# Performance work log

Measured on AMD Instinct MI355X. Metric: run time of the kernel, lower is better.

Reference implementation:

```python
import jax, jax.numpy as jnp
import numpy as np

B, T, N, F_IN = 32, 64, 128, 16
H, SOUT = 64, 16
D = N * SOUT            # transformer d_model = 2048
NHEADS, DH = 16, 128
DFF, LAYERS = 2048, 2
NCLASSES, OUT = 8, 10
THR = 0.004             # edge threshold on sigmoid(V)/N


def setup_inputs():
    key = jax.random.key(0)
    ks = iter(jax.random.split(key, 40))
    r = lambda *s: jax.random.normal(next(ks), s, jnp.float32) * 0.02
    return {
        'X': jax.random.normal(next(ks), (B, T, N * F_IN), jnp.float32),
        'V_Adap': jax.random.normal(next(ks), (NCLASSES, N, N), jnp.float32),
        'Wl': r(F_IN, H), 'bl': jnp.zeros((H,)),
        'Wr': r(F_IN, H), 'br': jnp.zeros((H,)),
        'att': jax.random.normal(next(ks), (H,), jnp.float32) * 0.1,
        'gat_bias': jnp.zeros((H,)),
        'Wfc': r(H, SOUT), 'bfc': jnp.zeros((SOUT,)),
        'Wq': r(LAYERS, D, D), 'bq': jnp.zeros((LAYERS, D)),
        'Wk': r(LAYERS, D, D), 'bk': jnp.zeros((LAYERS, D)),
        'Wv': r(LAYERS, D, D), 'bv': jnp.zeros((LAYERS, D)),
        'Wo': r(LAYERS, D, D), 'bo': jnp.zeros((LAYERS, D)),
        'ln1_g': jnp.ones((LAYERS, D)), 'ln1_b': jnp.zeros((LAYERS, D)),
        'W1': r(LAYERS, D, DFF), 'b1': jnp.zeros((LAYERS, DFF)),
        'W2': r(LAYERS, DFF, D), 'b2': jnp.zeros((LAYERS, D)),
        'ln2_g': jnp.ones((LAYERS, D)), 'ln2_b': jnp.zeros((LAYERS, D)),
        'Wout': r(D, OUT), 'bout': jnp.zeros((OUT,)),
        'class_idx': 2,
    }


def _ln(x, g, b):
    mu = jnp.mean(x, -1, keepdims=True)
    var = jnp.var(x, -1, keepdims=True)
    return (x - mu) / jnp.sqrt(var + 1e-5) * g + b


def reference(X, V_Adap, Wl, bl, Wr, br, att, gat_bias, Wfc, bfc,
              Wq, bq, Wk, bk, Wv, bv, Wo, bo, ln1_g, ln1_b,
              W1, b1, W2, b2, ln2_g, ln2_b, Wout, bout, class_idx):
    # dynamic adjacency: sigmoid + scale + threshold (data-dependent sparsity as a mask)
    A = jax.nn.sigmoid(V_Adap[class_idx]) / N
    mask = (A > THR) | jnp.eye(N, dtype=bool)   # GATv2Conv default add_self_loops

    def gat_step(x_t):                           # x_t: (B, N, F_IN)
        xl = x_t @ Wl + bl                       # source transform (B, N, H)
        xr = x_t @ Wr + br                       # target transform (B, N, H)
        s = jax.nn.leaky_relu(xl[:, :, None, :] + xr[:, None, :, :], 0.2)  # (B, src, dst, H)
        e = jnp.where(mask[None], jnp.einsum('bijh,h->bij', s, att), -1e9)
        alpha = jax.nn.softmax(e, axis=1)        # softmax over sources per target node
        out = jnp.einsum('bij,bih->bjh', alpha, xl) + gat_bias
        return out @ Wfc + bfc                   # (B, N, SOUT)

    Xr = X.reshape(B, T, N, F_IN).transpose(1, 0, 2, 3)   # (T, B, N, F)
    spatial = jax.lax.map(gat_step, Xr)                   # (T, B, N, SOUT)
    h = spatial.transpose(1, 0, 2, 3).reshape(B, T, D)

    # post-norm TransformerEncoder (torch defaults: relu, d_ff=2048, no dropout at eval)
    for l in range(LAYERS):
        q = (h @ Wq[l] + bq[l]).reshape(B, T, NHEADS, DH).transpose(0, 2, 1, 3)
        k = (h @ Wk[l] + bk[l]).reshape(B, T, NHEADS, DH).transpose(0, 2, 1, 3)
        v = (h @ Wv[l] + bv[l]).reshape(B, T, NHEADS, DH).transpose(0, 2, 1, 3)
        aw = jax.nn.softmax(jnp.einsum('bhqd,bhkd->bhqk', q, k) / np.float32(np.sqrt(DH)), axis=-1)
        ao = jnp.einsum('bhqk,bhkd->bhqd', aw, v).transpose(0, 2, 1, 3).reshape(B, T, D)
        h = _ln(h + ao @ Wo[l] + bo[l], ln1_g[l], ln1_b[l])
        ff = jax.nn.relu(h @ W1[l] + b1[l]) @ W2[l] + b2[l]
        h = _ln(h + ff, ln2_g[l], ln2_b[l])

    return h[:, -1, :] @ Wout + bout             # (B, OUT)
```

## Files before the change

### kernel.cpp

```cpp
#include <hip/hip_runtime.h>
#include <cstdint>
#include <cstddef>


typedef unsigned short u16;
typedef __bf16 bf16x8 __attribute__((ext_vector_type(8)));
typedef float f32x4 __attribute__((ext_vector_type(4)));
typedef unsigned int u32x4 __attribute__((ext_vector_type(4)));
typedef float f32x4v __attribute__((ext_vector_type(4)));
typedef unsigned short u16x4 __attribute__((ext_vector_type(4)));

__device__ __forceinline__ u16 f2b(float f) {
  union { float f; unsigned u; } x; x.f = f;
  unsigned r = x.u + 0x7fffu + ((x.u >> 16) & 1u);
  return (u16)(r >> 16);
}
__device__ __forceinline__ float b2f(u16 s) {
  union { unsigned u; float f; } x; x.u = ((unsigned)s) << 16;
  return x.f;
}
__device__ __forceinline__ float b2f_lo(unsigned q) {
  union { unsigned u; float f; } x; x.u = q << 16;
  return x.f;
}
__device__ __forceinline__ float b2f_hi(unsigned q) {
  union { unsigned u; float f; } x; x.u = q & 0xffff0000u;
  return x.f;
}

__device__ __forceinline__ void gload_lds16(const void* g, void* l) {
  __builtin_amdgcn_global_load_lds(
      (const __attribute__((address_space(1))) unsigned int*)g,
      (__attribute__((address_space(3))) unsigned int*)l, 16, 0, 0);
}

__global__ __launch_bounds__(1024) void gat_kernel(
    const float* __restrict__ X, const float* __restrict__ V_Adap,
    const int* __restrict__ class_idx,
    const float* __restrict__ Wl, const float* __restrict__ bl,
    const float* __restrict__ Wr, const float* __restrict__ br,
    const float* __restrict__ att, const float* __restrict__ gat_bias,
    const float* __restrict__ Wfc, const float* __restrict__ bfc,
    float* __restrict__ h_f32, u16* __restrict__ h_b16)
{
  const int bt = blockIdx.x;
  const int tid = threadIdx.x;

  __shared__ __align__(16) float xlT[64 * 132];
  __shared__ __align__(16) float xrT[64 * 132];
  __shared__ __align__(16) u16   xlTb[64 * 136];
  __shared__ __align__(16) u16   esbT[128 * 136];
  __shared__ __align__(16) u16   aggb[128 * 72];
  __shared__ __align__(16) float WlT[64 * 20];
  __shared__ __align__(16) float WrT[64 * 20];
  __shared__ __align__(16) float WfcT[16 * 66];
  __shared__ float atts[64], bls[64], brs[64], gbias[64], bfcs[16];
  __shared__ float cls[128], crs[128], inv_s[128];
  __shared__ float red[8 * 128];

  {
    const int h = tid >> 4, f = tid & 15;
    WlT[h * 20 + f] = Wl[f * 64 + h];
    WrT[h * 20 + f] = Wr[f * 64 + h];
    WfcT[f * 66 + h] = Wfc[h * 16 + f];
  }
  if (tid < 64) { atts[tid] = att[tid]; bls[tid] = bl[tid]; brs[tid] = br[tid]; gbias[tid] = gat_bias[tid]; }
  if (tid < 16) bfcs[tid] = bfc[tid];
  const int cidx = *class_idx;
  __syncthreads();

  {
    const int n = tid >> 3, hq = tid & 7;
    const float* xp = X + (size_t)bt * 2048 + n * 16;
    float xv[16];
    #pragma unroll
    for (int f4 = 0; f4 < 4; f4++) {
      f32x4v t4 = ((const f32x4v*)xp)[f4];
      xv[f4 * 4 + 0] = t4[0]; xv[f4 * 4 + 1] = t4[1];
      xv[f4 * 4 + 2] = t4[2]; xv[f4 * 4 + 3] = t4[3];
    }
    #pragma unroll
    for (int k = 0; k < 8; k++) {
      const int h = hq + 8 * k;
      float al = bls[h], ar = brs[h];
      #pragma unroll
      for (int f4 = 0; f4 < 4; f4++) {
        f32x4v wl = *(const f32x4v*)&WlT[h * 20 + f4 * 4];
        f32x4v wr = *(const f32x4v*)&WrT[h * 20 + f4 * 4];
        #pragma unroll
        for (int f = 0; f < 4; f++) {
          al = fmaf(xv[f4 * 4 + f], wl[f], al);
          ar = fmaf(xv[f4 * 4 + f], wr[f], ar);
        }
      }
      xlT[h * 132 + n] = al;
      xrT[h * 132 + n] = ar;
      xlTb[h * 136 + n] = f2b(al);
    }
  }
  __syncthreads();

  if (tid < 256) {
    const int n = tid & 127;
    const float* srcT = (tid < 128) ? xlT : xrT;
    float s = 0.f;
    for (int h = 0; h < 64; h++) s = fmaf(atts[h], srcT[h * 132 + n], s);
    if (tid < 128) cls[n] = s; else crs[n] = s;
  }
  __syncthreads();

  {
    const int i0 = (tid >> 5) * 4;
    const int j0 = (tid & 31) * 4;
    float acc[4][4] = {};
    #pragma unroll 2
    for (int h = 0; h < 64; h++) {
      const float ah = atts[h];
      f32x4v xa = *(const f32x4v*)&xlT[h * 132 + i0];
      f32x4v xb = *(const f32x4v*)&xrT[h * 132 + j0];
      #pragma unroll
      for (int a = 0; a < 4; a++)
        #pragma unroll
        for (int b = 0; b < 4; b++)
          acc[a][b] = fmaf(ah, __builtin_fabsf(xa[a] + xb[b]), acc[a][b]);
    }
    const float* Vc = V_Adap + (size_t)cidx * 16384;
    float vm[4][4];
    #pragma unroll
    for (int a = 0; a < 4; a++) {
      f32x4v vc = *(const f32x4v*)&Vc[(size_t)(i0 + a) * 128 + j0];
      #pragma unroll
      for (int b = 0; b < 4; b++) vm[a][b] = vc[b];
    }
    #pragma unroll
    for (int b = 0; b < 4; b++) {
      const int j = j0 + b;
      const float ej = 0.6f * crs[j];
      u16x4 pk;
      #pragma unroll
      for (int a = 0; a < 4; a++) {
        const int i = i0 + a;
        const float e = ej + 0.6f * cls[i] + 0.4f * acc[a][b];
        const bool m = (vm[a][b] > 0.04800922f) || (i == j);
        pk[a] = f2b(m ? e : -1e9f);
      }
      *(u16x4*)&esbT[j * 136 + i0] = pk;
    }
  }
  __syncthreads();

  {
    const int j = tid >> 3, c = tid & 7;
    u16* rp = &esbT[j * 136 + c * 16];
    float ps = 0.f;
    #pragma unroll
    for (int half = 0; half < 2; half++) {
      u32x4 q = *(u32x4*)(rp + half * 8);
      #pragma unroll
      for (int w2 = 0; w2 < 4; w2++) {
        const float p0 = __expf(b2f_lo(q[w2]));
        const float p1 = __expf(b2f_hi(q[w2]));
        ps += p0 + p1;
        q[w2] = (unsigned)f2b(p0) | ((unsigned)f2b(p1) << 16);
      }
      *(u32x4*)(rp + half * 8) = q;
    }
    red[c * 128 + j] = ps;
  }
  __syncthreads();
  if (tid < 128) {
    float s = 0.f;
    #pragma unroll
    for (int c = 0; c < 8; c++) s += red[c * 128 + tid];
    inv_s[tid] = 1.f / s;
  }
  __syncthreads();

  {
    const int w = tid >> 6, lane = tid & 63;
    const int lq = lane >> 4, lr = lane & 15;
    const int jt = w >> 1, ht0 = (w & 1) * 2;
    f32x4 acc2[2] = {};
    #pragma unroll
    for (int ks = 0; ks < 4; ks++) {
      const bf16x8 af = __builtin_bit_cast(bf16x8,
          *(const u32x4*)&esbT[(jt * 16 + lr) * 136 + ks * 32 + lq * 8]);
      #pragma unroll
      for (int t = 0; t < 2; t++) {
        const bf16x8 bfb = __builtin_bit_cast(bf16x8,
            *(const u32x4*)&xlTb[((ht0 + t) * 16 + lr) * 136 + ks * 32 + lq * 8]);
        acc2[t] = __builtin_amdgcn_mfma_f32_16x16x32_bf16(af, bfb, acc2[t], 0, 0, 0);
      }
    }
    #pragma unroll
    for (int t = 0; t < 2; t++) {
      const int h = (ht0 + t) * 16 + lr;
      const float gb = gbias[h];
      #pragma unroll
      for (int r = 0; r < 4; r++) {
        const int j = jt * 16 + lq * 4 + r;
        aggb[j * 72 + h] = f2b(acc2[t][r] * inv_s[j] + gb);
      }
    }
  }
  __syncthreads();

  {
    const int j = tid >> 3, s0 = (tid & 7) * 2;
    float o0 = bfcs[s0], o1 = bfcs[s0 + 1];
    #pragma unroll
    for (int h8 = 0; h8 < 8; h8++) {
      u32x4 q = *(const u32x4*)&aggb[j * 72 + h8 * 8];
      #pragma unroll
      for (int w2 = 0; w2 < 4; w2++) {
        const int h = h8 * 8 + w2 * 2;
        const float a0 = b2f_lo(q[w2]);
        const float a1 = b2f_hi(q[w2]);
        o0 = fmaf(a0, WfcT[s0 * 66 + h], o0);
        o1 = fmaf(a0, WfcT[(s0 + 1) * 66 + h], o1);
        o0 = fmaf(a1, WfcT[s0 * 66 + h + 1], o0);
        o1 = fmaf(a1, WfcT[(s0 + 1) * 66 + h + 1], o1);
      }
    }
    const size_t off = (size_t)bt * 2048 + j * 16 + s0;
    h_f32[off] = o0; h_f32[off + 1] = o1;
    h_b16[off] = f2b(o0); h_b16[off + 1] = f2b(o1);
  }
}

struct TransArgs {
  const float* s0; const float* s1; const float* s2;
  u16* d0; u16* d1; u16* d2;
};

__global__ __launch_bounds__(256) void transpose_cast(TransArgs p)
{
  const float* src = (blockIdx.z == 0) ? p.s0 : (blockIdx.z == 1) ? p.s1 : p.s2;
  u16* dst = (blockIdx.z == 0) ? p.d0 : (blockIdx.z == 1) ? p.d1 : p.d2;
  __shared__ u16 tile[64][66];
  const int k0 = blockIdx.y * 64, n0 = blockIdx.x * 64;
  const int tid = threadIdx.x;
  const int c = tid & 63, rb = tid >> 6;
  #pragma unroll
  for (int r = 0; r < 16; r++) {
    const int k = rb + r * 4;
    tile[k][c] = f2b(src[(size_t)(k0 + k) * 2048 + n0 + c]);
  }
  __syncthreads();
  #pragma unroll
  for (int r = 0; r < 16; r++) {
    const int n = rb + r * 4;
    dst[(size_t)(n0 + n) * 2048 + k0 + c] = tile[c][n];
  }
}

struct GemmArgs {
  const u16* A;
  const u16* Bt0; const u16* Bt1; const u16* Bt2;
  const float* b0; const float* b1; const float* b2;
  void* C0; void* C1; void* C2;
  int N; int K;
};

template <int MODE>
__global__ __launch_bounds__(256) void gemm_bt(GemmArgs g)
{
  const int z = blockIdx.z;
  const u16* Bt = (z == 0) ? g.Bt0 : (z == 1) ? g.Bt1 : g.Bt2;
  const float* bias = (z == 0) ? g.b0 : (z == 1) ? g.b1 : g.b2;
  void* C = (z == 0) ? g.C0 : (z == 1) ? g.C1 : g.C2;
  const int N = g.N, K = g.K;
  const int m0 = blockIdx.y * 128, n0 = blockIdx.x * 128;

  __shared__ __align__(16) u16 As[128 * 32];
  __shared__ __align__(16) u16 Bs[128 * 32];

  const int tid = threadIdx.x;
  const int lane = tid & 63, w = tid >> 6;
  const int srow = w * 16 + (lane >> 2);
  const int scol = (lane & 3) * 8;
  const u16* gA = g.A + (size_t)(m0 + srow) * K + scol;
  const u16* gB = Bt + (size_t)(n0 + srow) * K + scol;
  u16* lA0 = &As[(w * 16) * 32];
  u16* lA1 = &As[(64 + w * 16) * 32];
  u16* lB0 = &Bs[(w * 16) * 32];
  u16* lB1 = &Bs[(64 + w * 16) * 32];

  const int wm = (w >> 1) * 64, wn = (w & 1) * 64;
  const int lq = lane >> 4, lr = lane & 15;

  f32x4 acc[4][4] = {};

  for (int k0 = 0; k0 < K; k0 += 32) {
    gload_lds16(gA + k0, lA0);
    gload_lds16(gA + (size_t)64 * K + k0, lA1);
    gload_lds16(gB + k0, lB0);
    gload_lds16(gB + (size_t)64 * K + k0, lB1);
    __syncthreads();

    bf16x8 af[4], bf[4];
    #pragma unroll
    for (int i = 0; i < 4; i++) {
      af[i] = __builtin_bit_cast(bf16x8, *(const u32x4*)&As[(wm + i * 16 + lr) * 32 + lq * 8]);
      bf[i] = __builtin_bit_cast(bf16x8, *(const u32x4*)&Bs[(wn + i * 16 + lr) * 32 + lq * 8]);
    }
    #pragma unroll
    for (int mi = 0; mi < 4; mi++)
      #pragma unroll
      for (int ni = 0; ni < 4; ni++)
        acc[mi][ni] = __builtin_amdgcn_mfma_f32_16x16x32_bf16(af[mi], bf[ni], acc[mi][ni], 0, 0, 0);
    __syncthreads();
  }

  #pragma unroll
  for (int ni = 0; ni < 4; ni++) {
    const int col = n0 + wn + ni * 16 + lr;
    const float bv = bias[col];
    #pragma unroll
    for (int mi = 0; mi < 4; mi++) {
      #pragma unroll
      for (int r = 0; r < 4; r++) {
        const int row = m0 + wm + mi * 16 + lq * 4 + r;
        float v = acc[mi][ni][r] + bv;
        if (MODE == 0) {
          ((float*)C)[(size_t)row * N + col] = v;
        } else {
          if (MODE == 2) v = fmaxf(v, 0.f);
          ((u16*)C)[(size_t)row * N + col] = f2b(v);
        }
      }
    }
  }
}

template <int MODE>
__global__ __launch_bounds__(256) void gemm_bt64(GemmArgs g)
{
  const u16* Bt = g.Bt0;
  const float* bias = g.b0;
  void* C = g.C0;
  const int N = g.N, K = g.K;
  const int m0 = blockIdx.y * 128, n0 = blockIdx.x * 64;

  __shared__ __align__(16) u16 As[128 * 32];
  __shared__ __align__(16) u16 Bs[64 * 32];

  const int tid = threadIdx.x;
  const int lane = tid & 63, w = tid >> 6;
  const int srow = w * 16 + (lane >> 2);
  const int scol = (lane & 3) * 8;
  const u16* gA = g.A + (size_t)(m0 + srow) * K + scol;
  const u16* gB = Bt + (size_t)(n0 + srow) * K + scol;
  u16* lA0 = &As[(w * 16) * 32];
  u16* lA1 = &As[(64 + w * 16) * 32];
  u16* lB0 = &Bs[(w * 16) * 32];

  const int wm = w * 32;
  const int lq = lane >> 4, lr = lane & 15;

  f32x4 acc[2][4] = {};

  for (int k0 = 0; k0 < K; k0 += 32) {
    gload_lds16(gA + k0, lA0);
    gload_lds16(gA + (size_t)64 * K + k0, lA1);
    gload_lds16(gB + k0, lB0);
    __syncthreads();

    bf16x8 af[2], bf[4];
    #pragma unroll
    for (int i = 0; i < 2; i++)
      af[i] = __builtin_bit_cast(bf16x8, *(const u32x4*)&As[(wm + i * 16 + lr) * 32 + lq * 8]);
    #pragma unroll
    for (int i = 0; i < 4; i++)
      bf[i] = __builtin_bit_cast(bf16x8, *(const u32x4*)&Bs[(i * 16 + lr) * 32 + lq * 8]);
    #pragma unroll
    for (int mi = 0; mi < 2; mi++)
      #pragma unroll
      for (int ni = 0; ni < 4; ni++)
        acc[mi][ni] = __builtin_amdgcn_mfma_f32_16x16x32_bf16(af[mi], bf[ni], acc[mi][ni], 0, 0, 0);
    __syncthreads();
  }

  #pragma unroll
  for (int ni = 0; ni < 4; ni++) {
    const int col = n0 + ni * 16 + lr;
    const float bv = bias[col];
    #pragma unroll
    for (int mi = 0; mi < 2; mi++) {
      #pragma unroll
      for (int r = 0; r < 4; r++) {
        const int row = m0 + wm + mi * 16 + lq * 4 + r;
        float v = acc[mi][ni][r] + bv;
        if (MODE == 0) {
          ((float*)C)[(size_t)row * N + col] = v;
        } else {
          if (MODE == 2) v = fmaxf(v, 0.f);
          ((u16*)C)[(size_t)row * N + col] = f2b(v);
        }
      }
    }
  }
}

__global__ __launch_bounds__(256) void attn_kernel(
    const u16* __restrict__ Qb, const u16* __restrict__ Kb,
    const u16* __restrict__ Vb, u16* __restrict__ AOb)
{
  const int head = blockIdx.x, b = blockIdx.y;
  const int tid = threadIdx.x;
  __shared__ __align__(16) float qs[64 * 129];
  __shared__ __align__(16) float ks[64 * 129];
  __shared__ __align__(16) float vs[64 * 128];
  __shared__ __align__(16) float ss[64 * 65];
  const size_t base = ((size_t)b * 64) * 2048 + (size_t)head * 128;

  for (int idx = tid; idx < 8192; idx += 256) {
    const int t_ = idx >> 7, d = idx & 127;
    const size_t gp = base + (size_t)t_ * 2048 + d;
    qs[t_ * 129 + d] = b2f(Qb[gp]);
    ks[t_ * 129 + d] = b2f(Kb[gp]);
    vs[t_ * 128 + d] = b2f(Vb[gp]);
  }
  __syncthreads();

  {
    const int i0 = (tid >> 4) * 4, j0 = (tid & 15) * 4;
    float acc[4][4] = {};
    for (int d = 0; d < 128; d++) {
      float qv[4], kv[4];
      #pragma unroll
      for (int a = 0; a < 4; a++) qv[a] = qs[(i0 + a) * 129 + d];
      #pragma unroll
      for (int c = 0; c < 4; c++) kv[c] = ks[(j0 + c) * 129 + d];
      #pragma unroll
      for (int a = 0; a < 4; a++)
        #pragma unroll
        for (int c = 0; c < 4; c++)
          acc[a][c] = fmaf(qv[a], kv[c], acc[a][c]);
    }
    const float sc = 0.08838834764831845f;
    #pragma unroll
    for (int a = 0; a < 4; a++)
      #pragma unroll
      for (int c = 0; c < 4; c++)
        ss[(i0 + a) * 65 + j0 + c] = acc[a][c] * sc;
  }
  __syncthreads();

  if (tid < 64) {
    float mx = -3e38f;
    for (int j = 0; j < 64; j++) mx = fmaxf(mx, ss[tid * 65 + j]);
    float s = 0.f;
    for (int j = 0; j < 64; j++) {
      const float p = __expf(ss[tid * 65 + j] - mx);
      ss[tid * 65 + j] = p; s += p;
    }
    const float inv = 1.f / s;
    for (int j = 0; j < 64; j++) ss[tid * 65 + j] *= inv;
  }
  __syncthreads();

  {
    const int i0 = (tid >> 4) * 4, d0 = (tid & 15) * 8;
    float o[4][8] = {};
    for (int j = 0; j < 64; j++) {
      float pv[4];
      #pragma unroll
      for (int a = 0; a < 4; a++) pv[a] = ss[(i0 + a) * 65 + j];
      f32x4v v0 = *(const f32x4v*)&vs[j * 128 + d0];
      f32x4v v1 = *(const f32x4v*)&vs[j * 128 + d0 + 4];
      float vv[8] = {v0[0], v0[1], v0[2], v0[3], v1[0], v1[1], v1[2], v1[3]};
      #pragma unroll
      for (int a = 0; a < 4; a++)
        #pragma unroll
        for (int c = 0; c < 8; c++)
          o[a][c] = fmaf(pv[a], vv[c], o[a][c]);
    }
    #pragma unroll
    for (int a = 0; a < 4; a++)
      #pragma unroll
      for (int c = 0; c < 8; c++)
        AOb[base + (size_t)(i0 + a) * 2048 + d0 + c] = f2b(o[a][c]);
  }
}

__global__ __launch_bounds__(256) void ln_kernel(
    const float* __restrict__ hin, const float* __restrict__ delta,
    const float* __restrict__ gamma, const float* __restrict__ beta,
    float* __restrict__ hout, u16* __restrict__ bout_)
{
  const int token = blockIdx.x, tid = threadIdx.x;
  const size_t off = (size_t)token * 2048;
  __shared__ float red[8];
  float v[8];
  float s = 0.f;
  #pragma unroll
  for (int r = 0; r < 8; r++) {
    const int i = r * 256 + tid;
    v[r] = hin[off + i] + delta[off + i];
    s += v[r];
  }
  #pragma unroll
  for (int o = 32; o > 0; o >>= 1) s += __shfl_down(s, o, 64);
  if ((tid & 63) == 0) red[tid >> 6] = s;
  __syncthreads();
  const float mean = (red[0] + red[1] + red[2] + red[3]) * (1.f / 2048.f);
  float s2 = 0.f;
  #pragma unroll
  for (int r = 0; r < 8; r++) { const float d = v[r] - mean; s2 = fmaf(d, d, s2); }
  #pragma unroll
  for (int o = 32; o > 0; o >>= 1) s2 += __shfl_down(s2, o, 64);
  if ((tid & 63) == 0) red[4 + (tid >> 6)] = s2;
  __syncthreads();
  const float var = (red[4] + red[5] + red[6] + red[7]) * (1.f / 2048.f);
  const float rstd = rsqrtf(var + 1e-5f);
  #pragma unroll
  for (int r = 0; r < 8; r++) {
    const int i = r * 256 + tid;
    const float y = (v[r] - mean) * rstd * gamma[i] + beta[i];
    hout[off + i] = y;
    bout_[off + i] = f2b(y);
  }
}

__global__ __launch_bounds__(256) void final_kernel(
    const float* __restrict__ h, const float* __restrict__ Wout,
    const float* __restrict__ bout, float* __restrict__ out)
{
  const int b = blockIdx.x, tid = threadIdx.x;
  __shared__ float row[2048];
  __shared__ float part[256];
  const float* hr = h + ((size_t)b * 64 + 63) * 2048;
  for (int i = tid; i < 2048; i += 256) row[i] = hr[i];
  __syncthreads();
  const int o = tid & 15, ch = tid >> 4;
  float s = 0.f;
  if (o < 10) {
    const int i0 = ch * 128;
    for (int i = i0; i < i0 + 128; i++) s = fmaf(row[i], Wout[(size_t)i * 10 + o], s);
  }
  part[tid] = s;
  __syncthreads();
  if (tid < 10) {
    float t = bout[tid];
    for (int c2 = 0; c2 < 16; c2++) t += part[c2 * 16 + tid];
    out[(size_t)b * 10 + tid] = t;
  }
}

extern "C" void kernel_launch(void* const* d_in, const int* in_sizes, int n_in,
                              void* d_out, int out_size, void* d_ws, size_t ws_size,
                              hipStream_t stream)
{
  const float* X        = (const float*)d_in[0];
  const float* V_Adap   = (const float*)d_in[1];
  const float* Wl       = (const float*)d_in[2];
  const float* bl       = (const float*)d_in[3];
  const float* Wr       = (const float*)d_in[4];
  const float* br       = (const float*)d_in[5];
  const float* att      = (const float*)d_in[6];
  const float* gat_bias = (const float*)d_in[7];
  const float* Wfc      = (const float*)d_in[8];
  const float* bfc      = (const float*)d_in[9];
  const float* Wq       = (const float*)d_in[10];
  const float* bq       = (const float*)d_in[11];
  const float* Wk       = (const float*)d_in[12];
  const float* bk       = (const float*)d_in[13];
  const float* Wv       = (const float*)d_in[14];
  const float* bv       = (const float*)d_in[15];
  const float* Wo       = (const float*)d_in[16];
  const float* bo       = (const float*)d_in[17];
  const float* ln1_g    = (const float*)d_in[18];
  const float* ln1_b    = (const float*)d_in[19];
  const float* W1       = (const float*)d_in[20];
  const float* b1       = (const float*)d_in[21];
  const float* W2       = (const float*)d_in[22];
  const float* b2       = (const float*)d_in[23];
  const float* ln2_g    = (const float*)d_in[24];
  const float* ln2_b    = (const float*)d_in[25];
  const float* WoutP    = (const float*)d_in[26];
  const float* boutP    = (const float*)d_in[27];
  const int*   class_idx = (const int*)d_in[28];

  char* ws = (char*)d_ws;
  const size_t MB = (size_t)1 << 20;
  float* h_f32 = (float*)(ws);
  u16*   h_b16 = (u16*)(ws + 16 * MB);
  u16*   Qb    = (u16*)(ws + 24 * MB);
  u16*   Kb    = (u16*)(ws + 32 * MB);
  u16*   Vb    = (u16*)(ws + 40 * MB);
  u16*   AOb   = (u16*)(ws + 48 * MB);
  float* tmp   = (float*)(ws + 56 * MB);
  u16*   ff1b  = (u16*)(ws + 72 * MB);
  u16*   Wt0   = (u16*)(ws + 80 * MB);
  u16*   Wt1   = (u16*)(ws + 88 * MB);
  u16*   Wt2   = (u16*)(ws + 96 * MB);

  gat_kernel<<<2048, 1024, 0, stream>>>(X, V_Adap, class_idx, Wl, bl, Wr, br,
                                        att, gat_bias, Wfc, bfc, h_f32, h_b16);

  const size_t DD = 2048ull * 2048ull;
  for (int l = 0; l < 2; l++) {
    const size_t wofs = (size_t)l * DD;
    const size_t bofs = (size_t)l * 2048;

    transpose_cast<<<dim3(32, 32, 3), 256, 0, stream>>>(
        TransArgs{Wq + wofs, Wk + wofs, Wv + wofs, Wt0, Wt1, Wt2});
    gemm_bt<1><<<dim3(16, 16, 3), 256, 0, stream>>>(
        GemmArgs{h_b16, Wt0, Wt1, Wt2, bq + bofs, bk + bofs, bv + bofs,
                 Qb, Kb, Vb, 2048, 2048});

    attn_kernel<<<dim3(16, 32), 256, 0, stream>>>(Qb, Kb, Vb, AOb);

    transpose_cast<<<dim3(32, 32, 3), 256, 0, stream>>>(
        TransArgs{Wo + wofs, W1 + wofs, W2 + wofs, Wt0, Wt1, Wt2});

    gemm_bt64<0><<<dim3(32, 16), 256, 0, stream>>>(
        GemmArgs{AOb, Wt0, nullptr, nullptr, bo + bofs, nullptr, nullptr,
                 tmp, nullptr, nullptr, 2048, 2048});
    ln_kernel<<<2048, 256, 0, stream>>>(h_f32, tmp, ln1_g + bofs, ln1_b + bofs,
                                        h_f32, h_b16);

    gemm_bt64<2><<<dim3(32, 16), 256, 0, stream>>>(
        GemmArgs{h_b16, Wt1, nullptr, nullptr, b1 + bofs, nullptr, nullptr,
                 ff1b, nullptr, nullptr, 2048, 2048});

    gemm_bt64<0><<<dim3(32, 16), 256, 0, stream>>>(
        GemmArgs{ff1b, Wt2, nullptr, nullptr, b2 + bofs, nullptr, nullptr,
                 tmp, nullptr, nullptr, 2048, 2048});
    ln_kernel<<<2048, 256, 0, stream>>>(h_f32, tmp, ln2_g + bofs, ln2_b + bofs,
                                        h_f32, h_b16);
  }

  final_kernel<<<32, 256, 0, stream>>>(h_f32, WoutP, boutP, (float*)d_out);
}
```

Measured before the change: 966.4 us.

## Double-buffer GEMM LDS tiles with swizzle, vectorize attention and layernorm

Both bf16 GEMM kernels now double-buffer their LDS tiles, issuing the next K-tile's global-to-LDS loads before computing the current one. This removes one barrier per iteration and overlaps memory with MFMA work. Both also XOR-swizzle LDS columns to cut bank conflicts, and the 64-wide variant moves to K-tiles of 64. The attention kernel gets vectorized bf16 loads, float4 QK^T inner products, padding changed to 132, and a softmax spread over all 256 threads with shuffle reductions. The layernorm kernel uses float4 loads and stores. The cost is twice the LDS per GEMM block, which may reduce occupancy.

```diff
diff --git a/kernel.cpp b/kernel.cpp
--- a/kernel.cpp
+++ b/kernel.cpp
@@ -272,45 +272,58 @@
   const int N = g.N, K = g.K;
   const int m0 = blockIdx.y * 128, n0 = blockIdx.x * 128;
 
-  __shared__ __align__(16) u16 As[128 * 32];
-  __shared__ __align__(16) u16 Bs[128 * 32];
+  __shared__ __align__(16) u16 As[2][128 * 32];
+  __shared__ __align__(16) u16 Bs[2][128 * 32];
 
   const int tid = threadIdx.x;
   const int lane = tid & 63, w = tid >> 6;
   const int srow = w * 16 + (lane >> 2);
-  const int scol = (lane & 3) * 8;
+  const int scol = ((lane & 3) ^ ((lane >> 2) & 3)) * 8;
   const u16* gA = g.A + (size_t)(m0 + srow) * K + scol;
   const u16* gB = Bt + (size_t)(n0 + srow) * K + scol;
-  u16* lA0 = &As[(w * 16) * 32];
-  u16* lA1 = &As[(64 + w * 16) * 32];
-  u16* lB0 = &Bs[(w * 16) * 32];
-  u16* lB1 = &Bs[(64 + w * 16) * 32];
+  const int lbase = (w * 16) * 32;
 
   const int wm = (w >> 1) * 64, wn = (w & 1) * 64;
   const int lq = lane >> 4, lr = lane & 15;
+  const int csw = (lr & 3) << 3;
 
   f32x4 acc[4][4] = {};
-
-  for (int k0 = 0; k0 < K; k0 += 32) {
-    gload_lds16(gA + k0, lA0);
-    gload_lds16(gA + (size_t)64 * K + k0, lA1);
-    gload_lds16(gB + k0, lB0);
-    gload_lds16(gB + (size_t)64 * K + k0, lB1);
+  const int NT = K >> 5;
+
+  auto stage = [&](int buf, int kt) {
+    const int kk = kt << 5;
+    #pragma unroll
+    for (int c = 0; c < 2; c++) {
+      gload_lds16(gA + (size_t)(c * 64) * K + kk, &As[buf][lbase + c * 64 * 32]);
+      gload_lds16(gB + (size_t)(c * 64) * K + kk, &Bs[buf][lbase + c * 64 * 32]);
+    }
+  };
+  auto compute = [&](int buf) {
+    bf16x8 af[4], bfr[4];
+    #pragma unroll
+    for (int i = 0; i < 4; i++) {
+      af[i] = __builtin_bit_cast(bf16x8,
+          *(const u32x4*)&As[buf][(wm + i * 16 + lr) * 32 + ((lq * 8) ^ csw)]);
+      bfr[i] = __builtin_bit_cast(bf16x8,
+          *(const u32x4*)&Bs[buf][(wn + i * 16 + lr) * 32 + ((lq * 8) ^ csw)]);
+    }
+    #pragma unroll
+    for (int mi = 0; mi < 4; mi++)
+      #pragma unroll
+      for (int ni = 0; ni < 4; ni++)
+        acc[mi][ni] = __builtin_amdgcn_mfma_f32_16x16x32_bf16(af[mi], bfr[ni], acc[mi][ni], 0, 0, 0);
+  };
+
+  stage(0, 0);
+  __syncthreads();
+  int cur = 0;
+  for (int kt = 0; kt + 1 < NT; ++kt) {
+    stage(cur ^ 1, kt + 1);
+    compute(cur);
     __syncthreads();
-
-    bf16x8 af[4], bf[4];
-    #pragma unroll
-    for (int i = 0; i < 4; i++) {
-      af[i] = __builtin_bit_cast(bf16x8, *(const u32x4*)&As[(wm + i * 16 + lr) * 32 + lq * 8]);
-      bf[i] = __builtin_bit_cast(bf16x8, *(const u32x4*)&Bs[(wn + i * 16 + lr) * 32 + lq * 8]);
-    }
-    #pragma unroll
-    for (int mi = 0; mi < 4; mi++)
-      #pragma unroll
-      for (int ni = 0; ni < 4; ni++)
-        acc[mi][ni] = __builtin_amdgcn_mfma_f32_16x16x32_bf16(af[mi], bf[ni], acc[mi][ni], 0, 0, 0);
-    __syncthreads();
-  }
+    cur ^= 1;
+  }
+  compute(cur);
 
   #pragma unroll
   for (int ni = 0; ni < 4; ni++) {
@@ -342,44 +355,63 @@
   const int N = g.N, K = g.K;
   const int m0 = blockIdx.y * 128, n0 = blockIdx.x * 64;
 
-  __shared__ __align__(16) u16 As[128 * 32];
-  __shared__ __align__(16) u16 Bs[64 * 32];
+  __shared__ __align__(16) u16 As[2][128 * 64];
+  __shared__ __align__(16) u16 Bs[2][64 * 64];
 
   const int tid = threadIdx.x;
   const int lane = tid & 63, w = tid >> 6;
-  const int srow = w * 16 + (lane >> 2);
-  const int scol = (lane & 3) * 8;
+  const int srow = w * 8 + (lane >> 3);
+  const int scol = ((lane & 7) ^ (lane >> 3)) * 8;
   const u16* gA = g.A + (size_t)(m0 + srow) * K + scol;
   const u16* gB = Bt + (size_t)(n0 + srow) * K + scol;
-  u16* lA0 = &As[(w * 16) * 32];
-  u16* lA1 = &As[(64 + w * 16) * 32];
-  u16* lB0 = &Bs[(w * 16) * 32];
+  const int lbase = (w * 8) * 64;
 
   const int wm = w * 32;
   const int lq = lane >> 4, lr = lane & 15;
+  const int csw = (lr & 7) << 3;
 
   f32x4 acc[2][4] = {};
-
-  for (int k0 = 0; k0 < K; k0 += 32) {
-    gload_lds16(gA + k0, lA0);
-    gload_lds16(gA + (size_t)64 * K + k0, lA1);
-    gload_lds16(gB + k0, lB0);
+  const int NT = K >> 6;
+
+  auto stage = [&](int buf, int kt) {
+    const int kk = kt << 6;
+    #pragma unroll
+    for (int c = 0; c < 4; c++)
+      gload_lds16(gA + (size_t)(c * 32) * K + kk, &As[buf][lbase + c * 32 * 64]);
+    #pragma unroll
+    for (int c = 0; c < 2; c++)
+      gload_lds16(gB + (size_t)(c * 32) * K + kk, &Bs[buf][lbase + c * 32 * 64]);
+  };
+  auto compute = [&](int buf) {
+    #pragma unroll
+    for (int ks = 0; ks < 2; ks++) {
+      bf16x8 af[2], bfr[4];
+      #pragma unroll
+      for (int i = 0; i < 2; i++)
+        af[i] = __builtin_bit_cast(bf16x8,
+            *(const u32x4*)&As[buf][(wm + i * 16 + lr) * 64 + ((ks * 32 + lq * 8) ^ csw)]);
+      #pragma unroll
+      for (int i = 0; i < 4; i++)
+        bfr[i] = __builtin_bit_cast(bf16x8,
+            *(const u32x4*)&Bs[buf][(i * 16 + lr) * 64 + ((ks * 32 + lq * 8) ^ csw)]);
+      #pragma unroll
+      for (int mi = 0; mi < 2; mi++)
+        #pragma unroll
+        for (int ni = 0; ni < 4; ni++)
+          acc[mi][ni] = __builtin_amdgcn_mfma_f32_16x16x32_bf16(af[mi], bfr[ni], acc[mi][ni], 0, 0, 0);
+    }
+  };
+
+  stage(0, 0);
+  __syncthreads();
+  int cur = 0;
+  for (int kt = 0; kt + 1 < NT; ++kt) {
+    stage(cur ^ 1, kt + 1);
+    compute(cur);
     __syncthreads();
-
-    bf16x8 af[2], bf[4];
-    #pragma unroll
-    for (int i = 0; i < 2; i++)
-      af[i] = __builtin_bit_cast(bf16x8, *(const u32x4*)&As[(wm + i * 16 + lr) * 32 + lq * 8]);
-    #pragma unroll
-    for (int i = 0; i < 4; i++)
-      bf[i] = __builtin_bit_cast(bf16x8, *(const u32x4*)&Bs[(i * 16 + lr) * 32 + lq * 8]);
-    #pragma unroll
-    for (int mi = 0; mi < 2; mi++)
-      #pragma unroll
-      for (int ni = 0; ni < 4; ni++)
-        acc[mi][ni] = __builtin_amdgcn_mfma_f32_16x16x32_bf16(af[mi], bf[ni], acc[mi][ni], 0, 0, 0);
-    __syncthreads();
-  }
+    cur ^= 1;
+  }
+  compute(cur);
 
   #pragma unroll
   for (int ni = 0; ni < 4; ni++) {
@@ -408,55 +440,73 @@
 {
   const int head = blockIdx.x, b = blockIdx.y;
   const int tid = threadIdx.x;
-  __shared__ __align__(16) float qs[64 * 129];
-  __shared__ __align__(16) float ks[64 * 129];
+  __shared__ __align__(16) float qs[64 * 132];
+  __shared__ __align__(16) float ks[64 * 132];
   __shared__ __align__(16) float vs[64 * 128];
   __shared__ __align__(16) float ss[64 * 65];
   const size_t base = ((size_t)b * 64) * 2048 + (size_t)head * 128;
 
-  for (int idx = tid; idx < 8192; idx += 256) {
-    const int t_ = idx >> 7, d = idx & 127;
-    const size_t gp = base + (size_t)t_ * 2048 + d;
-    qs[t_ * 129 + d] = b2f(Qb[gp]);
-    ks[t_ * 129 + d] = b2f(Kb[gp]);
-    vs[t_ * 128 + d] = b2f(Vb[gp]);
-  }
-  __syncthreads();
-
-  {
-    const int i0 = (tid >> 4) * 4, j0 = (tid & 15) * 4;
+  for (int idx = tid; idx < 1024; idx += 256) {
+    const int t_ = idx >> 4, d8 = (idx & 15) * 8;
+    const size_t gp = base + (size_t)t_ * 2048 + d8;
+    const u32x4 q = *(const u32x4*)(Qb + gp);
+    const u32x4 k = *(const u32x4*)(Kb + gp);
+    const u32x4 v = *(const u32x4*)(Vb + gp);
+    f32x4 q0 = {b2f_lo(q[0]), b2f_hi(q[0]), b2f_lo(q[1]), b2f_hi(q[1])};
+    f32x4 q1 = {b2f_lo(q[2]), b2f_hi(q[2]), b2f_lo(q[3]), b2f_hi(q[3])};
+    f32x4 k0 = {b2f_lo(k[0]), b2f_hi(k[0]), b2f_lo(k[1]), b2f_hi(k[1])};
+    f32x4 k1 = {b2f_lo(k[2]), b2f_hi(k[2]), b2f_lo(k[3]), b2f_hi(k[3])};
+    f32x4 v0 = {b2f_lo(v[0]), b2f_hi(v[0]), b2f_lo(v[1]), b2f_hi(v[1])};
+    f32x4 v1 = {b2f_lo(v[2]), b2f_hi(v[2]), b2f_lo(v[3]), b2f_hi(v[3])};
+    *(f32x4*)&qs[t_ * 132 + d8] = q0; *(f32x4*)&qs[t_ * 132 + d8 + 4] = q1;
+    *(f32x4*)&ks[t_ * 132 + d8] = k0; *(f32x4*)&ks[t_ * 132 + d8 + 4] = k1;
+    *(f32x4*)&vs[t_ * 128 + d8] = v0; *(f32x4*)&vs[t_ * 128 + d8 + 4] = v1;
+  }
+  __syncthreads();
+
+  {
+    const int i0 = (tid >> 4) * 4, j0 = tid & 15;
     float acc[4][4] = {};
-    for (int d = 0; d < 128; d++) {
-      float qv[4], kv[4];
-      #pragma unroll
-      for (int a = 0; a < 4; a++) qv[a] = qs[(i0 + a) * 129 + d];
-      #pragma unroll
-      for (int c = 0; c < 4; c++) kv[c] = ks[(j0 + c) * 129 + d];
+    #pragma unroll 2
+    for (int d0 = 0; d0 < 128; d0 += 4) {
+      f32x4 qv[4], kv[4];
+      #pragma unroll
+      for (int a = 0; a < 4; a++) qv[a] = *(const f32x4*)&qs[(i0 + a) * 132 + d0];
+      #pragma unroll
+      for (int c = 0; c < 4; c++) kv[c] = *(const f32x4*)&ks[(j0 + c * 16) * 132 + d0];
       #pragma unroll
       for (int a = 0; a < 4; a++)
         #pragma unroll
         for (int c = 0; c < 4; c++)
-          acc[a][c] = fmaf(qv[a], kv[c], acc[a][c]);
+          #pragma unroll
+          for (int e = 0; e < 4; e++)
+            acc[a][c] = fmaf(qv[a][e], kv[c][e], acc[a][c]);
     }
     const float sc = 0.08838834764831845f;
     #pragma unroll
     for (int a = 0; a < 4; a++)
       #pragma unroll
       for (int c = 0; c < 4; c++)
-        ss[(i0 + a) * 65 + j0 + c] = acc[a][c] * sc;
-  }
-  __syncthreads();
-
-  if (tid < 64) {
+        ss[(i0 + a) * 65 + j0 + c * 16] = acc[a][c] * sc;
+  }
+  __syncthreads();
+
+  {
+    const int row = tid >> 2;
+    float* rp = &ss[row * 65 + (tid & 3) * 16];
     float mx = -3e38f;
-    for (int j = 0; j < 64; j++) mx = fmaxf(mx, ss[tid * 65 + j]);
+    #pragma unroll
+    for (int j = 0; j < 16; j++) mx = fmaxf(mx, rp[j]);
+    mx = fmaxf(mx, __shfl_xor(mx, 1, 64));
+    mx = fmaxf(mx, __shfl_xor(mx, 2, 64));
     float s = 0.f;
-    for (int j = 0; j < 64; j++) {
-      const float p = __expf(ss[tid * 65 + j] - mx);
-      ss[tid * 65 + j] = p; s += p;
-    }
+    #pragma unroll
+    for (int j = 0; j < 16; j++) { const float p = __expf(rp[j] - mx); rp[j] = p; s += p; }
+    s += __shfl_xor(s, 1, 64);
+    s += __shfl_xor(s, 2, 64);
     const float inv = 1.f / s;
-    for (int j = 0; j < 64; j++) ss[tid * 65 + j] *= inv;
+    #pragma unroll
+    for (int j = 0; j < 16; j++) rp[j] *= inv;
   }
   __syncthreads();
 
@@ -492,13 +542,15 @@
   const int token = blockIdx.x, tid = threadIdx.x;
   const size_t off = (size_t)token * 2048;
   __shared__ float red[8];
-  float v[8];
+  f32x4 v[2];
   float s = 0.f;
   #pragma unroll
-  for (int r = 0; r < 8; r++) {
-    const int i = r * 256 + tid;
-    v[r] = hin[off + i] + delta[off + i];
-    s += v[r];
+  for (int r = 0; r < 2; r++) {
+    const int i = r * 1024 + tid * 4;
+    const f32x4 a = *(const f32x4*)(hin + off + i);
+    const f32x4 b = *(const f32x4*)(delta + off + i);
+    v[r] = a + b;
+    s += v[r][0] + v[r][1] + v[r][2] + v[r][3];
   }
   #pragma unroll
   for (int o = 32; o > 0; o >>= 1) s += __shfl_down(s, o, 64);
@@ -507,7 +559,9 @@
   const float mean = (red[0] + red[1] + red[2] + red[3]) * (1.f / 2048.f);
   float s2 = 0.f;
   #pragma unroll
-  for (int r = 0; r < 8; r++) { const float d = v[r] - mean; s2 = fmaf(d, d, s2); }
+  for (int r = 0; r < 2; r++)
+    #pragma unroll
+    for (int e = 0; e < 4; e++) { const float d = v[r][e] - mean; s2 = fmaf(d, d, s2); }
   #pragma unroll
   for (int o = 32; o > 0; o >>= 1) s2 += __shfl_down(s2, o, 64);
   if ((tid & 63) == 0) red[4 + (tid >> 6)] = s2;
@@ -515,11 +569,19 @@
   const float var = (red[4] + red[5] + red[6] + red[7]) * (1.f / 2048.f);
   const float rstd = rsqrtf(var + 1e-5f);
   #pragma unroll
-  for (int r = 0; r < 8; r++) {
-    const int i = r * 256 + tid;
-    const float y = (v[r] - mean) * rstd * gamma[i] + beta[i];
-    hout[off + i] = y;
-    bout_[off + i] = f2b(y);
+  for (int r = 0; r < 2; r++) {
+    const int i = r * 1024 + tid * 4;
+    const f32x4 gm = *(const f32x4*)(gamma + i);
+    const f32x4 bt = *(const f32x4*)(beta + i);
+    f32x4 y;
+    u16x4 pb;
+    #pragma unroll
+    for (int e = 0; e < 4; e++) {
+      y[e] = (v[r][e] - mean) * rstd * gm[e] + bt[e];
+      pb[e] = f2b(y[e]);
+    }
+    *(f32x4*)(hout + off + i) = y;
+    *(u16x4*)(bout_ + off + i) = pb;
   }
 }
 
```

New measurement: 907.0 us. 6.1% less time.
